# Kernel tuning notes

Measured on AMD Instinct MI355X. Metric: run time of the kernel, lower is better.

## Reference

```python
import jax, jax.numpy as jnp
import numpy as np

N = 25000        # nodes
E = 400000       # edges (before self-loops)
HEADS = 8
GROUPS = 8
F_IN = 256
HID = 64
N_CLASS = 32
N_LAYERS = 3


def grouped_linear(x, w, b):
    # x: [..., Cin], w: [G, Cin//G, Cout//G], b: [Cout]
    G = w.shape[0]
    xs = x.reshape(x.shape[:-1] + (G, -1))
    out = jnp.einsum('...gi,gio->...go', xs, w)
    return out.reshape(x.shape[:-1] + (-1,)) + b


def gcn_norm(edge_index, n):
    # PyG gcn_norm with add_self_loops=True, unit edge weights
    row = jnp.concatenate([edge_index[0], jnp.arange(n)])
    col = jnp.concatenate([edge_index[1], jnp.arange(n)])
    w = jnp.ones(row.shape[0], jnp.float32)
    deg = jax.ops.segment_sum(w, col, num_segments=n)
    dis = jnp.where(deg > 0, jax.lax.rsqrt(deg), 0.0)
    return row, col, dis[row] * w * dis[col]


def dna_conv(x_all, row, col, norm, wq, bq, wk, bk, wv, bv):
    # x_all: [N, L, H]; row/col/norm: [E'] (edges incl. self-loops)
    Ee = row.shape[0]
    L, H = x_all.shape[1], x_all.shape[2]
    dh = H // HEADS
    # query from target's latest state, key/value from full source history
    q = grouped_linear(x_all[col, -1:], wq, bq).reshape(Ee, 1, HEADS, dh).transpose(0, 2, 1, 3)
    k = grouped_linear(x_all[row], wk, bk).reshape(Ee, L, HEADS, dh).transpose(0, 2, 1, 3)
    v = grouped_linear(x_all[row], wv, bv).reshape(Ee, L, HEADS, dh).transpose(0, 2, 1, 3)
    attn = jax.nn.softmax(jnp.einsum('ehqd,ehld->ehql', q, k) / jnp.sqrt(jnp.float32(dh)), axis=-1)
    out = jnp.einsum('ehql,ehld->ehqd', attn, v)           # [E', HEADS, 1, dh]
    out = out.transpose(0, 2, 1, 3).reshape(Ee, H)          # [E', H]
    return jax.ops.segment_sum(norm[:, None] * out, col, num_segments=N)


def setup_inputs() -> dict:
    key = jax.random.key(0)
    ks = jax.random.split(key, 12)
    s = 0.2
    return {
        'x': jax.random.normal(ks[0], (N, F_IN), jnp.float32),
        'edge_index': jax.random.randint(ks[1], (2, E), 0, N),
        'lin1_w': jax.random.normal(ks[2], (F_IN, HID), jnp.float32) * 0.05,
        'lin1_b': jnp.zeros((HID,), jnp.float32),
        'wq': jax.random.normal(ks[3], (N_LAYERS, GROUPS, HID // GROUPS, HID // GROUPS), jnp.float32) * s,
        'bq': jnp.zeros((N_LAYERS, HID), jnp.float32),
        'wk': jax.random.normal(ks[4], (N_LAYERS, GROUPS, HID // GROUPS, HID // GROUPS), jnp.float32) * s,
        'bk': jnp.zeros((N_LAYERS, HID), jnp.float32),
        'wv': jax.random.normal(ks[5], (N_LAYERS, GROUPS, HID // GROUPS, HID // GROUPS), jnp.float32) * s,
        'bv': jnp.zeros((N_LAYERS, HID), jnp.float32),
        'lin2_w': jax.random.normal(ks[6], (HID, N_CLASS), jnp.float32) * 0.1,
        'lin2_b': jnp.zeros((N_CLASS,), jnp.float32),
    }


def reference(x, edge_index, lin1_w, lin1_b, wq, bq, wk, bk, wv, bv, lin2_w, lin2_b):
    row, col, norm = gcn_norm(edge_index, N)
    h = jax.nn.relu(x @ lin1_w + lin1_b)                    # [N, HID]; dropout = identity (eval)
    x_all = h[:, None, :]                                   # [N, 1, HID]
    for l in range(N_LAYERS):
        out = jax.nn.relu(dna_conv(x_all, row, col, norm,
                                   wq[l], bq[l], wk[l], bk[l], wv[l], bv[l]))
        x_all = jnp.concatenate([x_all, out[:, None, :]], axis=1)
    logits = x_all[:, -1] @ lin2_w + lin2_b                 # [N, N_CLASS]
    return jax.nn.log_softmax(logits, axis=1)
```

## Files before the change

### kernel.cpp

```cpp
#include <hip/hip_runtime.h>
#include <hip/hip_fp16.h>
#include <math.h>

#define NN 25000
#define NE 400000
#define HID 64
#define F_IN 256
#define N_CLASS 32
#define MAXL 4
#define KVS 3
#define WPAD 264
#define SCAN_NB 98

typedef _Float16 f16;
typedef _Float16 f16x2 __attribute__((ext_vector_type(2)));
typedef _Float16 f16x8 __attribute__((ext_vector_type(8)));
typedef float f32x4 __attribute__((ext_vector_type(4)));

union F16x8 {
    f16x8 v;
    f16x2 h[4];
    __half2 hh[4];
};

__device__ __forceinline__ float dot2(f16x2 a, f16x2 b, float c) {
#if __has_builtin(__builtin_amdgcn_fdot2)
    return __builtin_amdgcn_fdot2(a, b, c, false);
#else
    return c + (float)a[0] * (float)b[0] + (float)a[1] * (float)b[1];
#endif
}

__global__ void deg_kernel(const int* __restrict__ col, int* __restrict__ deg, int E) {
    int e = blockIdx.x * blockDim.x + threadIdx.x;
    if (e < E) atomicAdd(&deg[col[e]], 1);
}

__global__ void scanA_kernel(const int* __restrict__ deg, int* __restrict__ bsum, int n) {
    int t = threadIdx.x;
    int i = blockIdx.x * 256 + t;
    int v = (i < n) ? deg[i] : 0;
    #pragma unroll
    for (int off = 1; off < 64; off <<= 1) v += __shfl_xor(v, off);
    __shared__ int wsum[4];
    if ((t & 63) == 0) wsum[t >> 6] = v;
    __syncthreads();
    if (t == 0) bsum[blockIdx.x] = wsum[0] + wsum[1] + wsum[2] + wsum[3];
}

__global__ void scanB_kernel(int* __restrict__ bsum, int nb) {
    __shared__ int s[128];
    int t = threadIdx.x;
    int v = (t < nb) ? bsum[t] : 0;
    s[t] = v;
    __syncthreads();
    for (int off = 1; off < 128; off <<= 1) {
        int u = (t >= off) ? s[t - off] : 0;
        __syncthreads();
        s[t] += u;
        __syncthreads();
    }
    if (t < nb) bsum[t] = s[t] - v;
}

__global__ void scanC_kernel(const int* __restrict__ deg, const int* __restrict__ bsum,
                             int* __restrict__ rowptr, int* __restrict__ cursor,
                             float* __restrict__ dis, int n) {
    int t = threadIdx.x;
    int i = blockIdx.x * 256 + t;
    int lane = t & 63, w = t >> 6;
    int v = (i < n) ? deg[i] : 0;
    int x = v;
    #pragma unroll
    for (int off = 1; off < 64; off <<= 1) {
        int u = __shfl_up(x, off);
        if (lane >= off) x += u;
    }
    __shared__ int wsum[4];
    if (lane == 63) wsum[w] = x;
    __syncthreads();
    int base = bsum[blockIdx.x];
    for (int ww = 0; ww < w; ++ww) base += wsum[ww];
    if (i < n) {
        int excl = base + x - v;
        rowptr[i] = excl;
        cursor[i] = excl;
        dis[i] = rsqrtf((float)(v + 1));
    }
}

__global__ void scatter_kernel(const int* __restrict__ row, const int* __restrict__ col,
                               int* __restrict__ cursor, int* __restrict__ csr_src, int E) {
    int e = blockIdx.x * blockDim.x + threadIdx.x;
    if (e >= E) return;
    int c = col[e];
    int p = atomicAdd(&cursor[c], 1);
    csr_src[p] = row[e];
}

__global__ void wprep_kernel(const float* __restrict__ w, f16* __restrict__ wt) {
    int e = blockIdx.x * blockDim.x + threadIdx.x;
    int k = e >> 6, nn = e & 63;
    wt[nn * F_IN + k] = (f16)w[e];
}

__global__ void __launch_bounds__(256) lin1_mfma_kernel(
        const float* __restrict__ x, const f16x8* __restrict__ wt,
        const float* __restrict__ b, float* __restrict__ x_all, int n) {
    __shared__ f16 wlds[64 * WPAD];
    int t = threadIdx.x;
    #pragma unroll
    for (int j = 0; j < 8; ++j) {
        int idx = t + j * 256;
        int e = idx * 8;
        int nr = e >> 8, k0 = e & 255;
        *(f16x8*)&wlds[nr * WPAD + k0] = wt[idx];
    }
    __syncthreads();
    int wave = t >> 6, lane = t & 63;
    int m = lane & 15, quad = lane >> 4;
    int rowA = blockIdx.x * 64 + wave * 16 + m;
    int rA = min(rowA, n - 1);
    const float* xp = x + (size_t)rA * F_IN + quad * 8;
    f32x4 acc[4] = {};
    for (int kk = 0; kk < F_IN; kk += 32) {
        float4 x0 = *(const float4*)(xp + kk);
        float4 x1 = *(const float4*)(xp + kk + 4);
        f16x8 a;
        a[0] = (f16)x0.x; a[1] = (f16)x0.y; a[2] = (f16)x0.z; a[3] = (f16)x0.w;
        a[4] = (f16)x1.x; a[5] = (f16)x1.y; a[6] = (f16)x1.z; a[7] = (f16)x1.w;
        #pragma unroll
        for (int nt = 0; nt < 4; ++nt) {
            f16x8 bf = *(const f16x8*)&wlds[(nt * 16 + m) * WPAD + kk + quad * 8];
            acc[nt] = __builtin_amdgcn_mfma_f32_16x16x32_f16(a, bf, acc[nt], 0, 0, 0);
        }
    }
    int rowC = blockIdx.x * 64 + wave * 16 + quad * 4;
    #pragma unroll
    for (int nt = 0; nt < 4; ++nt) {
        int col = nt * 16 + m;
        float bias = b[col];
        #pragma unroll
        for (int r = 0; r < 4; ++r) {
            int row = rowC + r;
            if (row < n)
                x_all[(size_t)row * (MAXL * HID) + col] = fmaxf(acc[nt][r] + bias, 0.f);
        }
    }
}

__global__ void transform_kernel(const float* __restrict__ x_all,
                                 const float* __restrict__ wq, const float* __restrict__ bq,
                                 const float* __restrict__ wk, const float* __restrict__ bk,
                                 const float* __restrict__ wv, const float* __restrict__ bv,
                                 const float* __restrict__ dis,
                                 f16x2* __restrict__ Q2, f16x2* __restrict__ KV,
                                 int n, int L) {
    int t = blockIdx.x * blockDim.x + threadIdx.x;
    int node = t >> 5, u = t & 31;
    if (node >= n) return;
    int g = u >> 2;
    int o0 = (u & 3) * 2;
    const float* xrow = x_all + (size_t)node * (MAXL * HID);
    float d = dis[node];

    {
        const float* xg = xrow + (L - 1) * HID + g * 8;
        const float* wg = wq + g * 64;
        float a0 = bq[g * 8 + o0], a1 = bq[g * 8 + o0 + 1];
        #pragma unroll
        for (int i = 0; i < 8; ++i) {
            float xv = xg[i];
            a0 = fmaf(xv, wg[i * 8 + o0], a0);
            a1 = fmaf(xv, wg[i * 8 + o0 + 1], a1);
        }
        f16x2 q; q[0] = (f16)a0; q[1] = (f16)a1;
        Q2[(size_t)node * 32 + u] = q;
    }
    for (int ll = 0; ll < L; ++ll) {
        const float* xg = xrow + ll * HID + g * 8;
        const float* wgk = wk + g * 64;
        const float* wgv = wv + g * 64;
        float k0 = bk[g * 8 + o0], k1 = bk[g * 8 + o0 + 1];
        float v0 = bv[g * 8 + o0], v1 = bv[g * 8 + o0 + 1];
        #pragma unroll
        for (int i = 0; i < 8; ++i) {
            float xv = xg[i];
            k0 = fmaf(xv, wgk[i * 8 + o0], k0);
            k1 = fmaf(xv, wgk[i * 8 + o0 + 1], k1);
            v0 = fmaf(xv, wgv[i * 8 + o0], v0);
            v1 = fmaf(xv, wgv[i * 8 + o0 + 1], v1);
        }
        f16x2 kh; kh[0] = (f16)k0; kh[1] = (f16)k1;
        f16x2 vh; vh[0] = (f16)(v0 * d); vh[1] = (f16)(v1 * d);
        size_t base = ((size_t)node * KVS + ll) * 2;
        KV[(base + 0) * 32 + u] = kh;
        KV[(base + 1) * 32 + u] = vh;
    }
}

template <int L>
__global__ void gather_kernel(const int* __restrict__ rowptr, const int* __restrict__ deg,
                              const int* __restrict__ csr_src, const float* __restrict__ dis,
                              const f16x8* __restrict__ Q8, const f16x8* __restrict__ KV8,
                              float* __restrict__ x_all, int n) {
    int wave = (int)((blockIdx.x * (size_t)blockDim.x + threadIdx.x) >> 6);
    int lane = threadIdx.x & 63;
    if (wave >= n) return;
    int c = wave;
    int u = lane & 7;
    int slot = lane >> 3;
    F16x8 q; q.v = Q8[(size_t)c * 8 + u];
    float nc = dis[c];
    int beg = rowptr[c];
    int dc = deg[c] + 1;
    float acc[8];
    #pragma unroll
    for (int i = 0; i < 8; ++i) acc[i] = 0.f;

    for (int j = 0; j < dc; j += 16) {
        int jj0 = j + slot;
        int jj1 = j + slot + 8;
        bool va0 = jj0 < dc, va1 = jj1 < dc;
        int r0 = c, r1 = c;
        if (va0 && jj0 > 0) r0 = csr_src[beg + jj0 - 1];
        if (va1)            r1 = csr_src[beg + jj1 - 1];

        F16x8 kk0[L], vv0[L], kk1[L], vv1[L];
        size_t rb0 = (size_t)r0 * (KVS * 2 * 8);
        size_t rb1 = (size_t)r1 * (KVS * 2 * 8);
        #pragma unroll
        for (int ll = 0; ll < L; ++ll) {
            kk0[ll].v = KV8[rb0 + ll * 16 + u];
            vv0[ll].v = KV8[rb0 + ll * 16 + 8 + u];
            kk1[ll].v = KV8[rb1 + ll * 16 + u];
            vv1[ll].v = KV8[rb1 + ll * 16 + 8 + u];
        }
        float s0[L], s1[L];
        #pragma unroll
        for (int ll = 0; ll < L; ++ll) {
            float p0 = 0.f, p1 = 0.f;
            #pragma unroll
            for (int i2 = 0; i2 < 4; ++i2) {
                p0 = dot2(q.h[i2], kk0[ll].h[i2], p0);
                p1 = dot2(q.h[i2], kk1[ll].h[i2], p1);
            }
            s0[ll] = p0 * 0.35355339059327373f;
            s1[ll] = p1 * 0.35355339059327373f;
        }
        float m0 = s0[0], m1 = s1[0];
        #pragma unroll
        for (int ll = 1; ll < L; ++ll) { m0 = fmaxf(m0, s0[ll]); m1 = fmaxf(m1, s1[ll]); }
        float sum0 = 0.f, sum1 = 0.f;
        #pragma unroll
        for (int ll = 0; ll < L; ++ll) {
            s0[ll] = __expf(s0[ll] - m0); sum0 += s0[ll];
            s1[ll] = __expf(s1[ll] - m1); sum1 += s1[ll];
        }
        float inv0 = va0 ? 1.f / sum0 : 0.f;
        float inv1 = va1 ? 1.f / sum1 : 0.f;

        __half2 ha[4];
        #pragma unroll
        for (int i2 = 0; i2 < 4; ++i2) ha[i2] = __float2half2_rn(0.f);
        #pragma unroll
        for (int ll = 0; ll < L; ++ll) {
            __half2 p0 = __float2half2_rn(s0[ll] * inv0);
            __half2 p1 = __float2half2_rn(s1[ll] * inv1);
            #pragma unroll
            for (int i2 = 0; i2 < 4; ++i2) {
                ha[i2] = __hfma2(p0, vv0[ll].hh[i2], ha[i2]);
                ha[i2] = __hfma2(p1, vv1[ll].hh[i2], ha[i2]);
            }
        }
        #pragma unroll
        for (int i2 = 0; i2 < 4; ++i2) {
            float2 f = __half22float2(ha[i2]);
            acc[i2 * 2]     += f.x;
            acc[i2 * 2 + 1] += f.y;
        }
    }
    #pragma unroll
    for (int off = 8; off < 64; off <<= 1) {
        #pragma unroll
        for (int i = 0; i < 8; ++i) acc[i] += __shfl_xor(acc[i], off);
    }
    if (slot == 0) {
        float4* dst = (float4*)(x_all + ((size_t)c * MAXL + L) * HID + u * 8);
        dst[0] = make_float4(fmaxf(acc[0] * nc, 0.f), fmaxf(acc[1] * nc, 0.f),
                             fmaxf(acc[2] * nc, 0.f), fmaxf(acc[3] * nc, 0.f));
        dst[1] = make_float4(fmaxf(acc[4] * nc, 0.f), fmaxf(acc[5] * nc, 0.f),
                             fmaxf(acc[6] * nc, 0.f), fmaxf(acc[7] * nc, 0.f));
    }
}

__global__ void final_kernel(const float* __restrict__ x_all, const float* __restrict__ w2,
                             const float* __restrict__ b2, float* __restrict__ out, int n) {
    int t = blockIdx.x * blockDim.x + threadIdx.x;
    int node = t >> 5;
    int o = t & 31;
    if (node >= n) return;
    const float* xr = x_all + (size_t)node * (MAXL * HID) + 3 * HID;
    float logit = b2[o];
    #pragma unroll
    for (int d = 0; d < HID; ++d) logit = fmaf(xr[d], w2[d * N_CLASS + o], logit);
    float m = logit;
    for (int off = 16; off; off >>= 1) m = fmaxf(m, __shfl_xor(m, off, 32));
    float e = expf(logit - m);
    float sum = e;
    for (int off = 16; off; off >>= 1) sum += __shfl_xor(sum, off, 32);
    out[(size_t)node * N_CLASS + o] = (logit - m) - logf(sum);
}

extern "C" void kernel_launch(void* const* d_in, const int* in_sizes, int n_in,
                              void* d_out, int out_size, void* d_ws, size_t ws_size,
                              hipStream_t stream) {
    const float* x      = (const float*)d_in[0];
    const int*   eidx   = (const int*)d_in[1];
    const float* lin1_w = (const float*)d_in[2];
    const float* lin1_b = (const float*)d_in[3];
    const float* wq     = (const float*)d_in[4];
    const float* bq     = (const float*)d_in[5];
    const float* wk     = (const float*)d_in[6];
    const float* bk     = (const float*)d_in[7];
    const float* wv     = (const float*)d_in[8];
    const float* bv     = (const float*)d_in[9];
    const float* lin2_w = (const float*)d_in[10];
    const float* lin2_b = (const float*)d_in[11];
    float* out = (float*)d_out;

    const int n  = NN;
    const int E  = NE;
    const int* row = eidx;
    const int* col = eidx + E;

    char* ws = (char*)d_ws;
    float*  x_all  = (float*)ws;   ws += (size_t)NN * MAXL * HID * 4;
    f16x2*  Q2     = (f16x2*)ws;   ws += (size_t)NN * 32 * 4;
    f16x2*  KV     = (f16x2*)ws;   ws += (size_t)NN * KVS * 2 * 32 * 4;
    float*  dis    = (float*)ws;   ws += (size_t)NN * 4;
    int*    deg    = (int*)ws;     ws += (size_t)NN * 4;
    int*    rowptr = (int*)ws;     ws += (size_t)NN * 4;
    int*    cursor = (int*)ws;     ws += (size_t)NN * 4;
    int*    csr    = (int*)ws;     ws += (size_t)NE * 4;
    f16*    wt16   = (f16*)ws;     ws += (size_t)HID * F_IN * 2;
    int*    bsum   = (int*)ws;     ws += 128 * 4;

    hipMemsetAsync(deg, 0, (size_t)NN * 4, stream);
    deg_kernel<<<(E + 255) / 256, 256, 0, stream>>>(col, deg, E);
    scanA_kernel<<<SCAN_NB, 256, 0, stream>>>(deg, bsum, n);
    scanB_kernel<<<1, 128, 0, stream>>>(bsum, SCAN_NB);
    scanC_kernel<<<SCAN_NB, 256, 0, stream>>>(deg, bsum, rowptr, cursor, dis, n);
    scatter_kernel<<<(E + 255) / 256, 256, 0, stream>>>(row, col, cursor, csr, E);
    wprep_kernel<<<(HID * F_IN + 255) / 256, 256, 0, stream>>>(lin1_w, wt16);

    lin1_mfma_kernel<<<(n + 63) / 64, 256, 0, stream>>>(x, (const f16x8*)wt16, lin1_b, x_all, n);

    for (int l = 0; l < 3; ++l) {
        int L = l + 1;
        transform_kernel<<<(n * 32 + 255) / 256, 256, 0, stream>>>(
            x_all, wq + l * 512, bq + l * 64, wk + l * 512, bk + l * 64,
            wv + l * 512, bv + l * 64, dis, Q2, KV, n, L);
        int blocks = (n + 3) / 4;
        if (L == 1)      gather_kernel<1><<<blocks, 256, 0, stream>>>(rowptr, deg, csr, dis, (const f16x8*)Q2, (const f16x8*)KV, x_all, n);
        else if (L == 2) gather_kernel<2><<<blocks, 256, 0, stream>>>(rowptr, deg, csr, dis, (const f16x8*)Q2, (const f16x8*)KV, x_all, n);
        else             gather_kernel<3><<<blocks, 256, 0, stream>>>(rowptr, deg, csr, dis, (const f16x8*)Q2, (const f16x8*)KV, x_all, n);
    }

    final_kernel<<<(n * N_CLASS + 255) / 256, 256, 0, stream>>>(x_all, lin2_w, lin2_b, out, n);
}
```

Baseline: 297.8 us.

## Prefetch next edge batch in gather, preload CSR indices per lane, fuse scanB

The gather kernel now loads up to 64 neighbor indices once per wave into lanes and hands them out with shuffles instead of repeated global loads. It also software-pipelines the edge loop, issuing the next 16-edge batch's K/V loads before processing the current batch to hide gather latency. Separately, the single-block scanB kernel is folded into scanC, where each block redoes the small block-sum scan, which removes one kernel launch. The prefetch doubles the live K/V registers and may lower occupancy.

```diff
diff --git a/kernel.cpp b/kernel.cpp
--- a/kernel.cpp
+++ b/kernel.cpp
@@ -48,25 +48,25 @@
     if (t == 0) bsum[blockIdx.x] = wsum[0] + wsum[1] + wsum[2] + wsum[3];
 }
 
-__global__ void scanB_kernel(int* __restrict__ bsum, int nb) {
-    __shared__ int s[128];
-    int t = threadIdx.x;
-    int v = (t < nb) ? bsum[t] : 0;
-    s[t] = v;
-    __syncthreads();
-    for (int off = 1; off < 128; off <<= 1) {
-        int u = (t >= off) ? s[t - off] : 0;
-        __syncthreads();
-        s[t] += u;
-        __syncthreads();
-    }
-    if (t < nb) bsum[t] = s[t] - v;
-}
-
 __global__ void scanC_kernel(const int* __restrict__ deg, const int* __restrict__ bsum,
                              int* __restrict__ rowptr, int* __restrict__ cursor,
                              float* __restrict__ dis, int n) {
+    __shared__ int s[128];
     int t = threadIdx.x;
+    {
+        int v = (t < SCAN_NB) ? bsum[t] : 0;
+        s[t] = v;
+        __syncthreads();
+        for (int off = 1; off < 128; off <<= 1) {
+            int u = (t >= off) ? s[t - off] : 0;
+            __syncthreads();
+            s[t] += u;
+            __syncthreads();
+        }
+    }
+    int base = (blockIdx.x > 0) ? s[blockIdx.x - 1] : 0;
+    __syncthreads();
+
     int i = blockIdx.x * 256 + t;
     int lane = t & 63, w = t >> 6;
     int v = (i < n) ? deg[i] : 0;
@@ -79,7 +79,6 @@
     __shared__ int wsum[4];
     if (lane == 63) wsum[w] = x;
     __syncthreads();
-    int base = bsum[blockIdx.x];
     for (int ww = 0; ww < w; ++ww) base += wsum[ww];
     if (i < n) {
         int excl = base + x - v;
@@ -214,28 +213,35 @@
     float nc = dis[c];
     int beg = rowptr[c];
     int dc = deg[c] + 1;
+    int r_lane = c;
+    if (lane > 0 && lane < dc) r_lane = csr_src[beg + lane - 1];
+
     float acc[8];
     #pragma unroll
     for (int i = 0; i < 8; ++i) acc[i] = 0.f;
 
-    for (int j = 0; j < dc; j += 16) {
-        int jj0 = j + slot;
-        int jj1 = j + slot + 8;
-        bool va0 = jj0 < dc, va1 = jj1 < dc;
+    F16x8 kk0[L], vv0[L], kk1[L], vv1[L];
+    bool va0, va1;
+
+    auto fetch = [&](int j, F16x8 (&k0)[L], F16x8 (&v0)[L],
+                     F16x8 (&k1)[L], F16x8 (&v1)[L], bool& a0, bool& a1) {
+        int jj0 = j + slot, jj1 = j + slot + 8;
+        a0 = jj0 < dc; a1 = jj1 < dc;
         int r0 = c, r1 = c;
-        if (va0 && jj0 > 0) r0 = csr_src[beg + jj0 - 1];
-        if (va1)            r1 = csr_src[beg + jj1 - 1];
-
-        F16x8 kk0[L], vv0[L], kk1[L], vv1[L];
+        if (a0) r0 = (jj0 < 64) ? __shfl(r_lane, jj0) : csr_src[beg + jj0 - 1];
+        if (a1) r1 = (jj1 < 64) ? __shfl(r_lane, jj1) : csr_src[beg + jj1 - 1];
         size_t rb0 = (size_t)r0 * (KVS * 2 * 8);
         size_t rb1 = (size_t)r1 * (KVS * 2 * 8);
         #pragma unroll
         for (int ll = 0; ll < L; ++ll) {
-            kk0[ll].v = KV8[rb0 + ll * 16 + u];
-            vv0[ll].v = KV8[rb0 + ll * 16 + 8 + u];
-            kk1[ll].v = KV8[rb1 + ll * 16 + u];
-            vv1[ll].v = KV8[rb1 + ll * 16 + 8 + u];
-        }
+            k0[ll].v = KV8[rb0 + ll * 16 + u];
+            v0[ll].v = KV8[rb0 + ll * 16 + 8 + u];
+            k1[ll].v = KV8[rb1 + ll * 16 + u];
+            v1[ll].v = KV8[rb1 + ll * 16 + 8 + u];
+        }
+    };
+
+    auto process = [&]() {
         float s0[L], s1[L];
         #pragma unroll
         for (int ll = 0; ll < L; ++ll) {
@@ -279,7 +285,26 @@
             acc[i2 * 2]     += f.x;
             acc[i2 * 2 + 1] += f.y;
         }
-    }
+    };
+
+    int iters = (dc + 15) >> 4;
+    fetch(0, kk0, vv0, kk1, vv1, va0, va1);
+    for (int it = 0; it < iters; ++it) {
+        F16x8 nk0[L], nv0[L], nk1[L], nv1[L];
+        bool na0 = false, na1 = false;
+        if (it + 1 < iters)
+            fetch((it + 1) * 16, nk0, nv0, nk1, nv1, na0, na1);
+        process();
+        if (it + 1 < iters) {
+            #pragma unroll
+            for (int ll = 0; ll < L; ++ll) {
+                kk0[ll] = nk0[ll]; vv0[ll] = nv0[ll];
+                kk1[ll] = nk1[ll]; vv1[ll] = nv1[ll];
+            }
+            va0 = na0; va1 = na1;
+        }
+    }
+
     #pragma unroll
     for (int off = 8; off < 64; off <<= 1) {
         #pragma unroll
@@ -349,7 +374,6 @@
     hipMemsetAsync(deg, 0, (size_t)NN * 4, stream);
     deg_kernel<<<(E + 255) / 256, 256, 0, stream>>>(col, deg, E);
     scanA_kernel<<<SCAN_NB, 256, 0, stream>>>(deg, bsum, n);
-    scanB_kernel<<<1, 128, 0, stream>>>(bsum, SCAN_NB);
     scanC_kernel<<<SCAN_NB, 256, 0, stream>>>(deg, bsum, rowptr, cursor, dis, n);
     scatter_kernel<<<(E + 255) / 256, 256, 0, stream>>>(row, col, cursor, csr, E);
     wprep_kernel<<<(HID * F_IN + 255) / 256, 256, 0, stream>>>(lin1_w, wt16);
```

Result: slower. 356.4 us (+19.7%).
